# Kernel tuning notes

Measured on AMD Instinct MI355X. Metric: run time of the kernel, lower is better.

## Reference

```python
import jax, jax.numpy as jnp
import numpy as np

TWO_PI = 2.0 * np.pi
SIGMA = 25.0  # marginal_prob_std sigma


def marginal_prob_std(t):
    # std(t) = sqrt((sigma^{2t} - 1) / (2 ln sigma)) for VE-SDE
    return jnp.sqrt((SIGMA ** (2.0 * t) - 1.0) / (2.0 * np.log(SIGMA)))


def edge_conv(x, src, dst, W1, b1, W2, b2, num_nodes):
    # PyG EdgeConv: msg = mlp(cat([x_i, x_j - x_i])), x_i = x[dst], x_j = x[src];
    # scatter-max over dst. First linear split so concat is never materialized:
    # cat([x_i, x_j - x_i]) @ W1 = x_i @ (Wa - Wb) + x_j @ Wb
    d = x.shape[-1]
    Wa, Wb = W1[:d], W1[d:]
    h_center = x @ (Wa - Wb)        # [N, H]
    h_nbr = x @ Wb                  # [N, H]
    e = jax.nn.relu(h_center[dst] + h_nbr[src] + b1)  # [E, H]
    e = e @ W2 + b2                 # [E, out]
    return jax.ops.segment_max(e, dst, num_segments=num_nodes)


def setup_inputs() -> dict:
    N, E, B, H, EM = 50000, 500000, 1024, 128, 64
    CLS, SD, GD, WD = 10, 4, 2, 2
    key = jax.random.key(0)
    ks = jax.random.split(key, 32)

    def lin(k, fi, fo):
        return jax.random.normal(k, (fi, fo), jnp.float32) / np.sqrt(fi)

    inp = {
        "t": jax.random.uniform(ks[0], (N, 1), jnp.float32, 1e-3, 1.0),
        "obj_x": jax.random.normal(ks[1], (N, SD), jnp.float32),
        "obj_geo": jax.random.normal(ks[2], (N, GD), jnp.float32),
        "wall": jax.random.normal(ks[3], (B, WD), jnp.float32),
        "category": jax.random.randint(ks[4], (N,), 0, CLS),
        "batch_idx": jnp.sort(jax.random.randint(ks[5], (N,), 0, B)),
        "src": jax.random.randint(ks[6], (E,), 0, N),
        "dst": jnp.tile(jnp.arange(N), E // N),  # every node receives edges
        "embed_W": jax.random.normal(ks[7], (CLS, EM), jnp.float32),
        "gfp_W": jax.random.normal(ks[8], (EM // 2,), jnp.float32) * 30.0,
        "sW": lin(ks[9], EM, EM), "sb": jnp.zeros((EM,), jnp.float32),
        "w1": lin(ks[10], WD, EM), "wb1": jnp.zeros((EM,), jnp.float32),
        "w2": lin(ks[11], EM, EM), "wb2": jnp.zeros((EM,), jnp.float32),
        "i1": lin(ks[12], SD + GD, H), "ib1": jnp.zeros((H,), jnp.float32),
        "i2": lin(ks[13], H, H), "ib2": jnp.zeros((H,), jnp.float32),
        "m1W1": lin(ks[14], 2 * (H + 3 * EM), H), "m1b1": jnp.zeros((H,), jnp.float32),
        "m1W2": lin(ks[15], H, H), "m1b2": jnp.zeros((H,), jnp.float32),
        "m2W1": lin(ks[16], 2 * (H + 3 * EM), H), "m2b1": jnp.zeros((H,), jnp.float32),
        "m2W2": lin(ks[17], H, SD), "m2b2": jnp.zeros((SD,), jnp.float32),
    }
    return inp


def reference(t, obj_x, obj_geo, wall, category, batch_idx, src, dst,
              embed_W, gfp_W, sW, sb, w1, wb1, w2, wb2,
              i1, ib1, i2, ib2, m1W1, m1b1, m1W2, m1b2,
              m2W1, m2b1, m2W2, m2b2):
    N = obj_x.shape[0]
    # conditioning features
    class_feat = jax.nn.relu(embed_W[category])                       # [N, EM]
    tv = t[:, 0]                                                      # [N]
    x_proj = tv[:, None] * gfp_W[None, :] * TWO_PI                    # [N, EM/2]
    gfp = jnp.concatenate([jnp.sin(x_proj), jnp.cos(x_proj)], axis=-1)
    sigma_feat = jax.nn.relu(gfp @ sW + sb)                           # [N, EM]
    wall_h = jax.nn.relu(jax.nn.relu(wall @ w1 + wb1) @ w2 + wb2)     # [B, EM]
    wall_feat = wall_h[batch_idx]                                     # [N, EM]
    cond = jnp.concatenate([class_feat, sigma_feat, wall_feat], axis=-1)

    # init encoder
    xin = jnp.concatenate([obj_x, obj_geo], axis=-1)                  # [N, 6]
    init = jax.nn.relu(jax.nn.relu(xin @ i1 + ib1) @ i2 + ib2)        # [N, H]

    # main backbone: two EdgeConvs with conditioning concat
    x = jnp.concatenate([init, cond], axis=-1)                        # [N, H+3EM]
    x = jax.nn.relu(edge_conv(x, src, dst, m1W1, m1b1, m1W2, m1b2, N))
    x = jnp.concatenate([x, cond], axis=-1)                           # [N, H+3EM]
    x = edge_conv(x, src, dst, m2W1, m2b1, m2W2, m2b2, N)             # [N, 4]

    return x / (marginal_prob_std(t) + 1e-7)
```

## Files before the change

kernel.cpp:

```cpp
#include <hip/hip_runtime.h>
#include <math.h>

#define NTHREADS 256
#define TWO_PI_F 6.28318530717958647692f
#define LOG_SIGMA 3.2188758248682006f

typedef unsigned short u16;
typedef unsigned int u32;
typedef _Float16 f16x2 __attribute__((ext_vector_type(2)));
typedef _Float16 f16x8 __attribute__((ext_vector_type(8)));
typedef float f32x4 __attribute__((ext_vector_type(4)));

#define MFMA16(a, b, c) __builtin_amdgcn_mfma_f32_16x16x32_f16((a), (b), (c), 0, 0, 0)

__device__ __forceinline__ u16 f2h(float f) {
  _Float16 h = (_Float16)f;
  union { _Float16 h; u16 u; } cv;
  cv.h = h;
  return cv.u;
}
__device__ __forceinline__ f16x2 relu2(f16x2 x) {
  f16x2 z;
  z[0] = (_Float16)0.f; z[1] = (_Float16)0.f;
  return __builtin_elementwise_max(x, z);
}

__global__ __launch_bounds__(256) void prep_kernel(
    const float* __restrict__ m1W2, const float* __restrict__ m1W1,
    const float* __restrict__ m2W1, const float* __restrict__ sW,
    const float* __restrict__ i1, const float* __restrict__ i2,
    const float* __restrict__ m2W2,
    u16* __restrict__ m1W2t, u16* __restrict__ Wc1t, u16* __restrict__ Wc2t,
    u16* __restrict__ sWt, u16* __restrict__ i1t, u16* __restrict__ i2t,
    u16* __restrict__ m2W2t) {
  int idx = blockIdx.x * 256 + threadIdx.x;
  if (idx < 16384) {
    int n = idx >> 7, k = idx & 127;
    m1W2t[idx] = f2h(m1W2[k * 128 + n]);
  } else if (idx < 98304) {
    int j = idx - 16384;
    int n = j / 320, k = j - n * 320;
    float v = (n < 128) ? (m1W1[k * 128 + n] - m1W1[(320 + k) * 128 + n])
                        : m1W1[(320 + k) * 128 + (n - 128)];
    Wc1t[j] = f2h(v);
  } else if (idx < 180224) {
    int j = idx - 98304;
    int n = j / 320, k = j - n * 320;
    float v = (n < 128) ? (m2W1[k * 128 + n] - m2W1[(320 + k) * 128 + n])
                        : m2W1[(320 + k) * 128 + (n - 128)];
    Wc2t[j] = f2h(v);
  } else if (idx < 184320) {
    int j = idx - 180224;
    int n = j >> 6, k = j & 63;
    sWt[j] = f2h(sW[k * 64 + n]);
  } else if (idx < 188416) {
    int j = idx - 184320;
    int n = j >> 5, k = j & 31;
    i1t[j] = (k < 6) ? f2h(i1[k * 128 + n]) : (u16)0;
  } else if (idx < 204800) {
    int j = idx - 188416;
    int n = j >> 7, k = j & 127;
    i2t[j] = f2h(i2[k * 128 + n]);
  } else if (idx < 205312) {
    int j = idx - 204800;
    int n = j >> 7, k = j & 127;
    m2W2t[j] = f2h(m2W2[k * 4 + n]);
  }
}

__global__ void wall_kernel(const float* __restrict__ wall,
                            const float* __restrict__ w1, const float* __restrict__ wb1,
                            const float* __restrict__ w2, const float* __restrict__ wb2,
                            float* __restrict__ wall_h) {
  __shared__ float h1[64];
  int b = blockIdx.x;
  int f = threadIdx.x;
  float v = wall[b * 2 + 0] * w1[f] + wall[b * 2 + 1] * w1[64 + f] + wb1[f];
  h1[f] = fmaxf(v, 0.f);
  __syncthreads();
  float acc = wb2[f];
  for (int k = 0; k < 64; ++k) acc = fmaf(h1[k], w2[k * 64 + f], acc);
  wall_h[b * 64 + f] = fmaxf(acc, 0.f);
}

__global__ __launch_bounds__(256) void node_kernel(
    const float* __restrict__ t, const float* __restrict__ obj_x,
    const float* __restrict__ obj_geo,
    const int* __restrict__ category, const int* __restrict__ batch_idx,
    const float* __restrict__ embed_W, const float* __restrict__ gfp_W,
    const u16* __restrict__ sWt, const float* __restrict__ sb,
    const u16* __restrict__ i1t, const float* __restrict__ ib1,
    const u16* __restrict__ i2t, const float* __restrict__ ib2,
    const u16* __restrict__ Wc1t, const float* __restrict__ m1b1,
    const float* __restrict__ wall_h,
    u16* __restrict__ hc1f, u16* __restrict__ hn1f,
    u16* __restrict__ cond_h, int N) {
  __shared__ u16 xb[64 * 328];
  __shared__ u16 ab[64 * 136];
  __shared__ float t_s[64];
  __shared__ int cat_s[64];
  __shared__ int bid_s[64];

  const int tid = threadIdx.x;
  const int base = blockIdx.x * 64;
  const int wave = tid >> 6, lane = tid & 63;
  const int ln16 = lane & 15, q8 = lane >> 4;

  f16x8 bs0 = *(const f16x8*)(sWt + (size_t)((wave * 16 + ln16) * 64) + q8 * 8);
  f16x8 bs1 = *(const f16x8*)(sWt + (size_t)((wave * 16 + ln16) * 64) + 32 + q8 * 8);
  f16x8 bh[2];
#pragma unroll
  for (int nt = 0; nt < 2; ++nt)
    bh[nt] = *(const f16x8*)(i1t + (size_t)((wave * 32 + nt * 16 + ln16) * 32) + q8 * 8);

  if (tid < 64) {
    int node = min(base + tid, N - 1);
    t_s[tid] = t[node];
    cat_s[tid] = category[node];
    bid_s[tid] = batch_idx[node];
  }
  __syncthreads();

  for (int idx = tid; idx < 64 * 32; idx += NTHREADS) {
    int row = idx >> 5, k = idx & 31;
    float xp = t_s[row] * gfp_W[k] * TWO_PI_F;
    float s, c;
    sincosf(xp, &s, &c);
    ab[row * 136 + k] = f2h(s);
    ab[row * 136 + 32 + k] = f2h(c);
  }
  for (int idx = tid; idx < 64 * 64; idx += NTHREADS) {
    int row = idx >> 6, f = idx & 63;
    xb[row * 328 + 128 + f] = f2h(fmaxf(embed_W[cat_s[row] * 64 + f], 0.f));
    xb[row * 328 + 256 + f] = f2h(wall_h[bid_s[row] * 64 + f]);
  }
  __syncthreads();

  f32x4 cs[4];
#pragma unroll
  for (int mt = 0; mt < 4; ++mt) cs[mt] = (f32x4)0.f;
#pragma unroll
  for (int mt = 0; mt < 4; ++mt) {
    f16x8 a0 = *(const f16x8*)&ab[(mt * 16 + ln16) * 136 + q8 * 8];
    cs[mt] = MFMA16(a0, bs0, cs[mt]);
  }
#pragma unroll
  for (int mt = 0; mt < 4; ++mt) {
    f16x8 a1 = *(const f16x8*)&ab[(mt * 16 + ln16) * 136 + 32 + q8 * 8];
    cs[mt] = MFMA16(a1, bs1, cs[mt]);
  }
  __syncthreads();

  {
    int col = wave * 16 + ln16;
    float bias = sb[col];
#pragma unroll
    for (int mt = 0; mt < 4; ++mt)
#pragma unroll
      for (int r = 0; r < 4; ++r)
        xb[(mt * 16 + q8 * 4 + r) * 328 + 192 + col] = f2h(fmaxf(cs[mt][r] + bias, 0.f));
  }
  for (int idx = tid; idx < 64 * 32; idx += NTHREADS) {
    int row = idx >> 5, k = idx & 31;
    int node = min(base + row, N - 1);
    float v = (k < 4) ? obj_x[node * 4 + k] : ((k < 6) ? obj_geo[node * 2 + (k - 4)] : 0.f);
    ab[row * 136 + k] = f2h(v);
  }
  __syncthreads();

  for (int idx = tid; idx < 64 * 24; idx += NTHREADS) {
    int row = idx / 24, q = idx - row * 24;
    int node = base + row;
    if (node < N)
      *(uint4*)&cond_h[(size_t)node * 192 + q * 8] = *(uint4*)&xb[row * 328 + 128 + q * 8];
  }

  f32x4 ch[2][4];
#pragma unroll
  for (int nt = 0; nt < 2; ++nt)
#pragma unroll
    for (int mt = 0; mt < 4; ++mt) ch[nt][mt] = (f32x4)0.f;
#pragma unroll
  for (int mt = 0; mt < 4; ++mt) {
    f16x8 a = *(const f16x8*)&ab[(mt * 16 + ln16) * 136 + q8 * 8];
#pragma unroll
    for (int nt = 0; nt < 2; ++nt) ch[nt][mt] = MFMA16(a, bh[nt], ch[nt][mt]);
  }
  f16x8 bcur2[2], bnext2[2];
#pragma unroll
  for (int nt = 0; nt < 2; ++nt)
    bcur2[nt] = *(const f16x8*)(i2t + (size_t)((wave * 32 + nt * 16 + ln16) * 128) + q8 * 8);
  __syncthreads();
#pragma unroll
  for (int nt = 0; nt < 2; ++nt) {
    int col = wave * 32 + nt * 16 + ln16;
    float bias = ib1[col];
#pragma unroll
    for (int mt = 0; mt < 4; ++mt)
#pragma unroll
      for (int r = 0; r < 4; ++r)
        ab[(mt * 16 + q8 * 4 + r) * 136 + col] = f2h(fmaxf(ch[nt][mt][r] + bias, 0.f));
  }
  __syncthreads();

  f32x4 ci[2][4];
#pragma unroll
  for (int nt = 0; nt < 2; ++nt)
#pragma unroll
    for (int mt = 0; mt < 4; ++mt) ci[nt][mt] = (f32x4)0.f;
  for (int kt = 0; kt < 4; ++kt) {
    if (kt < 3) {
#pragma unroll
      for (int nt = 0; nt < 2; ++nt)
        bnext2[nt] = *(const f16x8*)(i2t + (size_t)((wave * 32 + nt * 16 + ln16) * 128) +
                                     (kt + 1) * 32 + q8 * 8);
    }
#pragma unroll
    for (int mt = 0; mt < 4; ++mt) {
      f16x8 a = *(const f16x8*)&ab[(mt * 16 + ln16) * 136 + kt * 32 + q8 * 8];
#pragma unroll
      for (int nt = 0; nt < 2; ++nt) ci[nt][mt] = MFMA16(a, bcur2[nt], ci[nt][mt]);
    }
#pragma unroll
    for (int nt = 0; nt < 2; ++nt) bcur2[nt] = bnext2[nt];
  }
#pragma unroll
  for (int nt = 0; nt < 2; ++nt) {
    int col = wave * 32 + nt * 16 + ln16;
    float bias = ib2[col];
#pragma unroll
    for (int mt = 0; mt < 4; ++mt)
#pragma unroll
      for (int r = 0; r < 4; ++r)
        xb[(mt * 16 + q8 * 4 + r) * 328 + col] = f2h(fmaxf(ci[nt][mt][r] + bias, 0.f));
  }
  __syncthreads();

  f32x4 c2[4][4];
#pragma unroll
  for (int nt = 0; nt < 4; ++nt)
#pragma unroll
    for (int mt = 0; mt < 4; ++mt) c2[nt][mt] = (f32x4)0.f;
  f16x8 bcur[4], bnext[4];
#pragma unroll
  for (int nt = 0; nt < 4; ++nt)
    bcur[nt] = *(const f16x8*)(Wc1t + (size_t)((wave * 64 + nt * 16 + ln16) * 320) + q8 * 8);
  for (int kt = 0; kt < 10; ++kt) {
    if (kt < 9) {
#pragma unroll
      for (int nt = 0; nt < 4; ++nt)
        bnext[nt] = *(const f16x8*)(Wc1t + (size_t)((wave * 64 + nt * 16 + ln16) * 320) +
                                    (kt + 1) * 32 + q8 * 8);
    }
#pragma unroll
    for (int mt = 0; mt < 4; ++mt) {
      f16x8 a = *(const f16x8*)&xb[(mt * 16 + ln16) * 328 + kt * 32 + q8 * 8];
#pragma unroll
      for (int nt = 0; nt < 4; ++nt) c2[nt][mt] = MFMA16(a, bcur[nt], c2[nt][mt]);
    }
#pragma unroll
    for (int nt = 0; nt < 4; ++nt) bcur[nt] = bnext[nt];
  }
#pragma unroll
  for (int nt = 0; nt < 4; ++nt) {
    int col = wave * 64 + nt * 16 + ln16;
#pragma unroll
    for (int mt = 0; mt < 4; ++mt)
#pragma unroll
      for (int r = 0; r < 4; ++r) {
        int node = base + mt * 16 + q8 * 4 + r;
        if (node < N) {
          if (col < 128)
            hc1f[(size_t)node * 128 + col] = f2h(c2[nt][mt][r] + m1b1[col]);
          else
            hn1f[(size_t)node * 128 + (col - 128)] = f2h(c2[nt][mt][r]);
        }
      }
  }
}

__global__ __launch_bounds__(256) void edge1_kernel(
    const u16* __restrict__ hc1f, const u16* __restrict__ hn1f,
    const int* __restrict__ src, const u16* __restrict__ m1W2t,
    const float* __restrict__ m1b2, u16* __restrict__ y, int N) {
  __shared__ int sid[320];
  const int tid = threadIdx.x;
  const int base = blockIdx.x * 32;
  const int wave = tid >> 6, lane = tid & 63;
  const int ln16 = lane & 15, q8 = lane >> 4;
  const int rowoff = (wave >> 1) * 16;
  const int colh = (wave & 1) * 64;
  const int myrow = rowoff + ln16;
  const int mynode = min(base + myrow, N - 1);

  for (int idx = tid; idx < 320; idx += NTHREADS) {
    int e = idx >> 5, n = idx & 31;
    sid[idx] = src[min(base + n, N - 1) + e * N];
  }

  uint4 hc4[4];
#pragma unroll
  for (int kt = 0; kt < 4; ++kt)
    hc4[kt] = *(const uint4*)&hc1f[(size_t)mynode * 128 + kt * 32 + q8 * 8];

  f16x8 bfr[4][4];
#pragma unroll
  for (int nt = 0; nt < 4; ++nt)
#pragma unroll
    for (int kt = 0; kt < 4; ++kt)
      bfr[nt][kt] = *(const f16x8*)(m1W2t + (size_t)(colh + nt * 16 + ln16) * 128 +
                                    kt * 32 + q8 * 8);
  __syncthreads();

  f32x4 ymax[4];
#pragma unroll
  for (int nt = 0; nt < 4; ++nt)
#pragma unroll
    for (int r = 0; r < 4; ++r) ymax[nt][r] = -3.0e38f;

  uint4 g[2][4];
  {
    int s0 = sid[myrow];
    int s1 = sid[32 + myrow];
#pragma unroll
    for (int kt = 0; kt < 4; ++kt) {
      g[0][kt] = *(const uint4*)&hn1f[(size_t)s0 * 128 + kt * 32 + q8 * 8];
      g[1][kt] = *(const uint4*)&hn1f[(size_t)s1 * 128 + kt * 32 + q8 * 8];
    }
  }
#pragma unroll
  for (int e = 0; e < 10; ++e) {
    const int sl = e & 1;
    uint4 a4[4];
#pragma unroll
    for (int kt = 0; kt < 4; ++kt) {
      f16x2* ap = (f16x2*)&a4[kt];
      const f16x2* gp = (const f16x2*)&g[sl][kt];
      const f16x2* hp = (const f16x2*)&hc4[kt];
#pragma unroll
      for (int p = 0; p < 4; ++p) ap[p] = relu2(gp[p] + hp[p]);
    }
    if (e + 2 < 10) {
      int s = sid[(e + 2) * 32 + myrow];
#pragma unroll
      for (int kt = 0; kt < 4; ++kt)
        g[sl][kt] = *(const uint4*)&hn1f[(size_t)s * 128 + kt * 32 + q8 * 8];
    }
    f32x4 c[4];
#pragma unroll
    for (int nt = 0; nt < 4; ++nt) c[nt] = (f32x4)0.f;
#pragma unroll
    for (int kt = 0; kt < 4; ++kt) {
      f16x8 a = *(const f16x8*)&a4[kt];
#pragma unroll
      for (int nt = 0; nt < 4; ++nt) c[nt] = MFMA16(a, bfr[nt][kt], c[nt]);
    }
#pragma unroll
    for (int nt = 0; nt < 4; ++nt)
#pragma unroll
      for (int r = 0; r < 4; ++r) ymax[nt][r] = fmaxf(ymax[nt][r], c[nt][r]);
  }

#pragma unroll
  for (int nt = 0; nt < 4; ++nt) {
    int col = colh + nt * 16 + ln16;
    float bias = m1b2[col];
#pragma unroll
    for (int r = 0; r < 4; ++r) {
      int node = base + rowoff + q8 * 4 + r;
      if (node < N) y[(size_t)node * 128 + col] = f2h(fmaxf(ymax[nt][r] + bias, 0.f));
    }
  }
}

__global__ __launch_bounds__(256) void conv2_kernel(
    const u16* __restrict__ y, const u16* __restrict__ cond_h,
    const u16* __restrict__ Wc2t, const float* __restrict__ m2b1,
    u16* __restrict__ hc2f, u16* __restrict__ hn2f, int N) {
  __shared__ u16 xb[64 * 328];
  const int tid = threadIdx.x;
  const int base = blockIdx.x * 64;
  const int wave = tid >> 6, lane = tid & 63;
  const int ln16 = lane & 15, q8 = lane >> 4;

  for (int idx = tid; idx < 64 * 16; idx += NTHREADS) {
    int row = idx >> 4, q = idx & 15;
    int nd = min(base + row, N - 1);
    *(uint4*)&xb[row * 328 + q * 8] = *(const uint4*)&y[(size_t)nd * 128 + q * 8];
  }
  for (int idx = tid; idx < 64 * 24; idx += NTHREADS) {
    int row = idx / 24, q = idx - row * 24;
    int nd = min(base + row, N - 1);
    *(uint4*)&xb[row * 328 + 128 + q * 8] = *(const uint4*)&cond_h[(size_t)nd * 192 + q * 8];
  }
  __syncthreads();

  f32x4 c2[4][4];
#pragma unroll
  for (int nt = 0; nt < 4; ++nt)
#pragma unroll
    for (int mt = 0; mt < 4; ++mt) c2[nt][mt] = (f32x4)0.f;
  f16x8 bcur[4], bnext[4];
#pragma unroll
  for (int nt = 0; nt < 4; ++nt)
    bcur[nt] = *(const f16x8*)(Wc2t + (size_t)((wave * 64 + nt * 16 + ln16) * 320) + q8 * 8);
  for (int kt = 0; kt < 10; ++kt) {
    if (kt < 9) {
#pragma unroll
      for (int nt = 0; nt < 4; ++nt)
        bnext[nt] = *(const f16x8*)(Wc2t + (size_t)((wave * 64 + nt * 16 + ln16) * 320) +
                                    (kt + 1) * 32 + q8 * 8);
    }
#pragma unroll
    for (int mt = 0; mt < 4; ++mt) {
      f16x8 a = *(const f16x8*)&xb[(mt * 16 + ln16) * 328 + kt * 32 + q8 * 8];
#pragma unroll
      for (int nt = 0; nt < 4; ++nt) c2[nt][mt] = MFMA16(a, bcur[nt], c2[nt][mt]);
    }
#pragma unroll
    for (int nt = 0; nt < 4; ++nt) bcur[nt] = bnext[nt];
  }
#pragma unroll
  for (int nt = 0; nt < 4; ++nt) {
    int col = wave * 64 + nt * 16 + ln16;
#pragma unroll
    for (int mt = 0; mt < 4; ++mt)
#pragma unroll
      for (int r = 0; r < 4; ++r) {
        int node = base + mt * 16 + q8 * 4 + r;
        if (node < N) {
          if (col < 128)
            hc2f[(size_t)node * 128 + col] = f2h(c2[nt][mt][r] + m2b1[col]);
          else
            hn2f[(size_t)node * 128 + (col - 128)] = f2h(c2[nt][mt][r]);
        }
      }
  }
}

__global__ __launch_bounds__(256) void edge2_kernel(
    const u16* __restrict__ hc2f, const u16* __restrict__ hn2f,
    const int* __restrict__ src, const float* __restrict__ t,
    const u16* __restrict__ m2W2t, const float* __restrict__ m2b2,
    float* __restrict__ out, int N) {
  const int tid = threadIdx.x;
  const int base = blockIdx.x * 32;
  const int ln = tid >> 3, kq = tid & 7;
  const int node = min(base + ln, N - 1);

  uint4 hc0 = *(const uint4*)&hc2f[(size_t)node * 128 + kq * 16];
  uint4 hc1_ = *(const uint4*)&hc2f[(size_t)node * 128 + kq * 16 + 8];
  uint4 w4[4][2];
#pragma unroll
  for (int j = 0; j < 4; ++j) {
    w4[j][0] = *(const uint4*)&m2W2t[j * 128 + kq * 16];
    w4[j][1] = *(const uint4*)&m2W2t[j * 128 + kq * 16 + 8];
  }
  float ymax[4] = {-3.0e38f, -3.0e38f, -3.0e38f, -3.0e38f};

  uint4 g[2][2];
  {
    int s0 = src[node];
    int s1 = src[node + N];
    g[0][0] = *(const uint4*)&hn2f[(size_t)s0 * 128 + kq * 16];
    g[0][1] = *(const uint4*)&hn2f[(size_t)s0 * 128 + kq * 16 + 8];
    g[1][0] = *(const uint4*)&hn2f[(size_t)s1 * 128 + kq * 16];
    g[1][1] = *(const uint4*)&hn2f[(size_t)s1 * 128 + kq * 16 + 8];
  }
#pragma unroll
  for (int e = 0; e < 10; ++e) {
    const int sl = e & 1;
    f16x2 a2[8];
    {
      const f16x2* gp0 = (const f16x2*)&g[sl][0];
      const f16x2* gp1 = (const f16x2*)&g[sl][1];
      const f16x2* hp0 = (const f16x2*)&hc0;
      const f16x2* hp1 = (const f16x2*)&hc1_;
#pragma unroll
      for (int p = 0; p < 4; ++p) a2[p] = relu2(gp0[p] + hp0[p]);
#pragma unroll
      for (int p = 0; p < 4; ++p) a2[4 + p] = relu2(gp1[p] + hp1[p]);
    }
    if (e + 2 < 10) {
      int s = src[node + (e + 2) * N];
      g[sl][0] = *(const uint4*)&hn2f[(size_t)s * 128 + kq * 16];
      g[sl][1] = *(const uint4*)&hn2f[(size_t)s * 128 + kq * 16 + 8];
    }
    float acc[4] = {0.f, 0.f, 0.f, 0.f};
#pragma unroll
    for (int j = 0; j < 4; ++j) {
      const f16x2* wp0 = (const f16x2*)&w4[j][0];
      const f16x2* wp1 = (const f16x2*)&w4[j][1];
#pragma unroll
      for (int p = 0; p < 4; ++p) {
        acc[j] = __builtin_amdgcn_fdot2(a2[p], wp0[p], acc[j], false);
        acc[j] = __builtin_amdgcn_fdot2(a2[4 + p], wp1[p], acc[j], false);
      }
    }
#pragma unroll
    for (int mask = 1; mask <= 4; mask <<= 1)
#pragma unroll
      for (int j = 0; j < 4; ++j) acc[j] += __shfl_xor(acc[j], mask);
#pragma unroll
    for (int j = 0; j < 4; ++j) ymax[j] = fmaxf(ymax[j], acc[j]);
  }
  if (kq < 4 && base + ln < N) {
    float tv = t[node];
    float mps = sqrtf((expf(2.f * tv * LOG_SIGMA) - 1.f) * (1.f / (2.f * LOG_SIGMA)));
    out[(size_t)node * 4 + kq] = (ymax[kq] + m2b2[kq]) / (mps + 1e-7f);
  }
}

extern "C" void kernel_launch(void* const* d_in, const int* in_sizes, int n_in,
                              void* d_out, int out_size, void* d_ws, size_t ws_size,
                              hipStream_t stream) {
  const float* t = (const float*)d_in[0];
  const float* obj_x = (const float*)d_in[1];
  const float* obj_geo = (const float*)d_in[2];
  const float* wall = (const float*)d_in[3];
  const int* category = (const int*)d_in[4];
  const int* batch_idx = (const int*)d_in[5];
  const int* src = (const int*)d_in[6];
  const float* embed_W = (const float*)d_in[8];
  const float* gfp_W = (const float*)d_in[9];
  const float* sW = (const float*)d_in[10];
  const float* sb = (const float*)d_in[11];
  const float* w1 = (const float*)d_in[12];
  const float* wb1 = (const float*)d_in[13];
  const float* w2 = (const float*)d_in[14];
  const float* wb2 = (const float*)d_in[15];
  const float* i1 = (const float*)d_in[16];
  const float* ib1 = (const float*)d_in[17];
  const float* i2 = (const float*)d_in[18];
  const float* ib2 = (const float*)d_in[19];
  const float* m1W1 = (const float*)d_in[20];
  const float* m1b1 = (const float*)d_in[21];
  const float* m1W2 = (const float*)d_in[22];
  const float* m1b2 = (const float*)d_in[23];
  const float* m2W1 = (const float*)d_in[24];
  const float* m2b1 = (const float*)d_in[25];
  const float* m2W2 = (const float*)d_in[26];
  const float* m2b2 = (const float*)d_in[27];
  float* out = (float*)d_out;

  const int N = in_sizes[0];
  const int B = in_sizes[3] / 2;

  char* w = (char*)d_ws;
  float* wall_h = (float*)w; w += (size_t)B * 64 * 4;
  u16* cond_h = (u16*)w;    w += (size_t)N * 192 * 2;
  u16* hc1f = (u16*)w;      w += (size_t)N * 128 * 2;
  u16* hn1f = (u16*)w;      w += (size_t)N * 128 * 2;
  u16* hc2f = (u16*)w;      w += (size_t)N * 128 * 2;
  u16* hn2f = (u16*)w;      w += (size_t)N * 128 * 2;
  u16* yb = (u16*)w;        w += (size_t)N * 128 * 2;
  u16* m1W2t = (u16*)w;     w += (size_t)128 * 128 * 2;
  u16* Wc1t = (u16*)w;      w += (size_t)256 * 320 * 2;
  u16* Wc2t = (u16*)w;      w += (size_t)256 * 320 * 2;
  u16* sWt = (u16*)w;       w += (size_t)64 * 64 * 2;
  u16* i1t = (u16*)w;       w += (size_t)128 * 32 * 2;
  u16* i2t = (u16*)w;       w += (size_t)128 * 128 * 2;
  u16* m2W2t = (u16*)w;     w += (size_t)4 * 128 * 2;

  prep_kernel<<<dim3(802), dim3(256), 0, stream>>>(m1W2, m1W1, m2W1, sW, i1, i2, m2W2,
                                                   m1W2t, Wc1t, Wc2t, sWt, i1t, i2t, m2W2t);
  wall_kernel<<<dim3(B), dim3(64), 0, stream>>>(wall, w1, wb1, w2, wb2, wall_h);
  node_kernel<<<dim3((N + 63) / 64), dim3(NTHREADS), 0, stream>>>(
      t, obj_x, obj_geo, category, batch_idx, embed_W, gfp_W, sWt, sb,
      i1t, ib1, i2t, ib2, Wc1t, m1b1, wall_h, hc1f, hn1f, cond_h, N);
  edge1_kernel<<<dim3((N + 31) / 32), dim3(NTHREADS), 0, stream>>>(
      hc1f, hn1f, src, m1W2t, m1b2, yb, N);
  conv2_kernel<<<dim3((N + 63) / 64), dim3(NTHREADS), 0, stream>>>(
      yb, cond_h, Wc2t, m2b1, hc2f, hn2f, N);
  edge2_kernel<<<dim3((N + 31) / 32), dim3(NTHREADS), 0, stream>>>(
      hc2f, hn2f, src, t, m2W2t, m2b2, out, N);
}
```

Before: 332.6 us.

## Use MFMA in edge2 and retile edge1 to 16 nodes per block

Edge2's per-edge 128x4 projection moves from fdot2 with cross-lane shuffle reductions to a 16x16x32 MFMA. The weights are zero-padded to 16 output columns and the source indices are staged in shared memory for 64 nodes per block. Edge1 now handles 16 nodes per block, with each wave owning 32 output columns, and both kernels get a launch_bounds occupancy hint. This cuts shuffle and VALU work and raises occupancy. The costs are wasted MFMA columns in edge2 and each hn1f gathered row being loaded by all four waves in edge1.

After: 359.4 us. +8.1%, slower.

```diff
diff --git a/kernel.cpp b/kernel.cpp
--- a/kernel.cpp
+++ b/kernel.cpp
@@ -61,10 +61,10 @@
     int j = idx - 188416;
     int n = j >> 7, k = j & 127;
     i2t[j] = f2h(i2[k * 128 + n]);
-  } else if (idx < 205312) {
+  } else if (idx < 206848) {
     int j = idx - 204800;
     int n = j >> 7, k = j & 127;
-    m2W2t[j] = f2h(m2W2[k * 4 + n]);
+    m2W2t[j] = (n < 4) ? f2h(m2W2[k * 4 + n]) : (u16)0;
   }
 }
 
@@ -279,22 +279,19 @@
   }
 }
 
-__global__ __launch_bounds__(256) void edge1_kernel(
+__global__ __launch_bounds__(256, 4) void edge1_kernel(
     const u16* __restrict__ hc1f, const u16* __restrict__ hn1f,
     const int* __restrict__ src, const u16* __restrict__ m1W2t,
     const float* __restrict__ m1b2, u16* __restrict__ y, int N) {
-  __shared__ int sid[320];
+  __shared__ int sid[160];
   const int tid = threadIdx.x;
-  const int base = blockIdx.x * 32;
+  const int base = blockIdx.x * 16;
   const int wave = tid >> 6, lane = tid & 63;
   const int ln16 = lane & 15, q8 = lane >> 4;
-  const int rowoff = (wave >> 1) * 16;
-  const int colh = (wave & 1) * 64;
-  const int myrow = rowoff + ln16;
-  const int mynode = min(base + myrow, N - 1);
-
-  for (int idx = tid; idx < 320; idx += NTHREADS) {
-    int e = idx >> 5, n = idx & 31;
+  const int mynode = min(base + ln16, N - 1);
+
+  for (int idx = tid; idx < 160; idx += NTHREADS) {
+    int e = idx >> 4, n = idx & 15;
     sid[idx] = src[min(base + n, N - 1) + e * N];
   }
 
@@ -303,25 +300,25 @@
   for (int kt = 0; kt < 4; ++kt)
     hc4[kt] = *(const uint4*)&hc1f[(size_t)mynode * 128 + kt * 32 + q8 * 8];
 
-  f16x8 bfr[4][4];
-#pragma unroll
-  for (int nt = 0; nt < 4; ++nt)
+  f16x8 bfr[2][4];
+#pragma unroll
+  for (int nt = 0; nt < 2; ++nt)
 #pragma unroll
     for (int kt = 0; kt < 4; ++kt)
-      bfr[nt][kt] = *(const f16x8*)(m1W2t + (size_t)(colh + nt * 16 + ln16) * 128 +
+      bfr[nt][kt] = *(const f16x8*)(m1W2t + (size_t)(wave * 32 + nt * 16 + ln16) * 128 +
                                     kt * 32 + q8 * 8);
   __syncthreads();
 
-  f32x4 ymax[4];
-#pragma unroll
-  for (int nt = 0; nt < 4; ++nt)
+  f32x4 ymax[2];
+#pragma unroll
+  for (int nt = 0; nt < 2; ++nt)
 #pragma unroll
     for (int r = 0; r < 4; ++r) ymax[nt][r] = -3.0e38f;
 
   uint4 g[2][4];
   {
-    int s0 = sid[myrow];
-    int s1 = sid[32 + myrow];
+    int s0 = sid[ln16];
+    int s1 = sid[16 + ln16];
 #pragma unroll
     for (int kt = 0; kt < 4; ++kt) {
       g[0][kt] = *(const uint4*)&hn1f[(size_t)s0 * 128 + kt * 32 + q8 * 8];
@@ -341,33 +338,33 @@
       for (int p = 0; p < 4; ++p) ap[p] = relu2(gp[p] + hp[p]);
     }
     if (e + 2 < 10) {
-      int s = sid[(e + 2) * 32 + myrow];
+      int s = sid[(e + 2) * 16 + ln16];
 #pragma unroll
       for (int kt = 0; kt < 4; ++kt)
         g[sl][kt] = *(const uint4*)&hn1f[(size_t)s * 128 + kt * 32 + q8 * 8];
     }
-    f32x4 c[4];
-#pragma unroll
-    for (int nt = 0; nt < 4; ++nt) c[nt] = (f32x4)0.f;
+    f32x4 c[2];
+#pragma unroll
+    for (int nt = 0; nt < 2; ++nt) c[nt] = (f32x4)0.f;
 #pragma unroll
     for (int kt = 0; kt < 4; ++kt) {
       f16x8 a = *(const f16x8*)&a4[kt];
 #pragma unroll
-      for (int nt = 0; nt < 4; ++nt) c[nt] = MFMA16(a, bfr[nt][kt], c[nt]);
-    }
-#pragma unroll
-    for (int nt = 0; nt < 4; ++nt)
+      for (int nt = 0; nt < 2; ++nt) c[nt] = MFMA16(a, bfr[nt][kt], c[nt]);
+    }
+#pragma unroll
+    for (int nt = 0; nt < 2; ++nt)
 #pragma unroll
       for (int r = 0; r < 4; ++r) ymax[nt][r] = fmaxf(ymax[nt][r], c[nt][r]);
   }
 
 #pragma unroll
-  for (int nt = 0; nt < 4; ++nt) {
-    int col = colh + nt * 16 + ln16;
+  for (int nt = 0; nt < 2; ++nt) {
+    int col = wave * 32 + nt * 16 + ln16;
     float bias = m1b2[col];
 #pragma unroll
     for (int r = 0; r < 4; ++r) {
-      int node = base + rowoff + q8 * 4 + r;
+      int node = base + q8 * 4 + r;
       if (node < N) y[(size_t)node * 128 + col] = f2h(fmaxf(ymax[nt][r] + bias, 0.f));
     }
   }
@@ -438,76 +435,88 @@
   }
 }
 
-__global__ __launch_bounds__(256) void edge2_kernel(
+__global__ __launch_bounds__(256, 4) void edge2_kernel(
     const u16* __restrict__ hc2f, const u16* __restrict__ hn2f,
     const int* __restrict__ src, const float* __restrict__ t,
     const u16* __restrict__ m2W2t, const float* __restrict__ m2b2,
     float* __restrict__ out, int N) {
+  __shared__ int sid[640];
   const int tid = threadIdx.x;
-  const int base = blockIdx.x * 32;
-  const int ln = tid >> 3, kq = tid & 7;
-  const int node = min(base + ln, N - 1);
-
-  uint4 hc0 = *(const uint4*)&hc2f[(size_t)node * 128 + kq * 16];
-  uint4 hc1_ = *(const uint4*)&hc2f[(size_t)node * 128 + kq * 16 + 8];
-  uint4 w4[4][2];
-#pragma unroll
-  for (int j = 0; j < 4; ++j) {
-    w4[j][0] = *(const uint4*)&m2W2t[j * 128 + kq * 16];
-    w4[j][1] = *(const uint4*)&m2W2t[j * 128 + kq * 16 + 8];
-  }
-  float ymax[4] = {-3.0e38f, -3.0e38f, -3.0e38f, -3.0e38f};
-
-  uint4 g[2][2];
+  const int base = blockIdx.x * 64;
+  const int wave = tid >> 6, lane = tid & 63;
+  const int ln16 = lane & 15, q8 = lane >> 4;
+  const int myrow = wave * 16 + ln16;
+  const int mynode = min(base + myrow, N - 1);
+
+  for (int idx = tid; idx < 640; idx += NTHREADS) {
+    int e = idx >> 6, n = idx & 63;
+    sid[idx] = src[min(base + n, N - 1) + e * N];
+  }
+
+  uint4 hc4[4];
+#pragma unroll
+  for (int kt = 0; kt < 4; ++kt)
+    hc4[kt] = *(const uint4*)&hc2f[(size_t)mynode * 128 + kt * 32 + q8 * 8];
+
+  f16x8 bfr[4];
+#pragma unroll
+  for (int kt = 0; kt < 4; ++kt)
+    bfr[kt] = *(const f16x8*)(m2W2t + (size_t)ln16 * 128 + kt * 32 + q8 * 8);
+  __syncthreads();
+
+  f32x4 ymax;
+#pragma unroll
+  for (int r = 0; r < 4; ++r) ymax[r] = -3.0e38f;
+
+  uint4 g[2][4];
   {
-    int s0 = src[node];
-    int s1 = src[node + N];
-    g[0][0] = *(const uint4*)&hn2f[(size_t)s0 * 128 + kq * 16];
-    g[0][1] = *(const uint4*)&hn2f[(size_t)s0 * 128 + kq * 16 + 8];
-    g[1][0] = *(const uint4*)&hn2f[(size_t)s1 * 128 + kq * 16];
-    g[1][1] = *(const uint4*)&hn2f[(size_t)s1 * 128 + kq * 16 + 8];
+    int s0 = sid[myrow];
+    int s1 = sid[64 + myrow];
+#pragma unroll
+    for (int kt = 0; kt < 4; ++kt) {
+      g[0][kt] = *(const uint4*)&hn2f[(size_t)s0 * 128 + kt * 32 + q8 * 8];
+      g[1][kt] = *(const uint4*)&hn2f[(size_t)s1 * 128 + kt * 32 + q8 * 8];
+    }
   }
 #pragma unroll
   for (int e = 0; e < 10; ++e) {
     const int sl = e & 1;
-    f16x2 a2[8];
-    {
-      const f16x2* gp0 = (const f16x2*)&g[sl][0];
-      const f16x2* gp1 = (const f16x2*)&g[sl][1];
-      const f16x2* hp0 = (const f16x2*)&hc0;
-      const f16x2* hp1 = (const f16x2*)&hc1_;
-#pragma unroll
-      for (int p = 0; p < 4; ++p) a2[p] = relu2(gp0[p] + hp0[p]);
-#pragma unroll
-      for (int p = 0; p < 4; ++p) a2[4 + p] = relu2(gp1[p] + hp1[p]);
+    uint4 a4[4];
+#pragma unroll
+    for (int kt = 0; kt < 4; ++kt) {
+      f16x2* ap = (f16x2*)&a4[kt];
+      const f16x2* gp = (const f16x2*)&g[sl][kt];
+      const f16x2* hp = (const f16x2*)&hc4[kt];
+#pragma unroll
+      for (int p = 0; p < 4; ++p) ap[p] = relu2(gp[p] + hp[p]);
     }
     if (e + 2 < 10) {
-      int s = src[node + (e + 2) * N];
-      g[sl][0] = *(const uint4*)&hn2f[(size_t)s * 128 + kq * 16];
-      g[sl][1] = *(const uint4*)&hn2f[(size_t)s * 128 + kq * 16 + 8];
-    }
-    float acc[4] = {0.f, 0.f, 0.f, 0.f};
-#pragma unroll
-    for (int j = 0; j < 4; ++j) {
-      const f16x2* wp0 = (const f16x2*)&w4[j][0];
-      const f16x2* wp1 = (const f16x2*)&w4[j][1];
-#pragma unroll
-      for (int p = 0; p < 4; ++p) {
-        acc[j] = __builtin_amdgcn_fdot2(a2[p], wp0[p], acc[j], false);
-        acc[j] = __builtin_amdgcn_fdot2(a2[4 + p], wp1[p], acc[j], false);
+      int s = sid[(e + 2) * 64 + myrow];
+#pragma unroll
+      for (int kt = 0; kt < 4; ++kt)
+        g[sl][kt] = *(const uint4*)&hn2f[(size_t)s * 128 + kt * 32 + q8 * 8];
+    }
+    f32x4 c = (f32x4)0.f;
+#pragma unroll
+    for (int kt = 0; kt < 4; ++kt) {
+      f16x8 a = *(const f16x8*)&a4[kt];
+      c = MFMA16(a, bfr[kt], c);
+    }
+#pragma unroll
+    for (int r = 0; r < 4; ++r) ymax[r] = fmaxf(ymax[r], c[r]);
+  }
+
+  if (ln16 < 4) {
+    float bias = m2b2[ln16];
+#pragma unroll
+    for (int r = 0; r < 4; ++r) {
+      int node = base + wave * 16 + q8 * 4 + r;
+      if (node < N) {
+        float tv = t[node];
+        float mps = sqrtf((expf(2.f * tv * LOG_SIGMA) - 1.f) * (1.f / (2.f * LOG_SIGMA)));
+        out[(size_t)node * 4 + ln16] = (ymax[r] + bias) / (mps + 1e-7f);
       }
     }
-#pragma unroll
-    for (int mask = 1; mask <= 4; mask <<= 1)
-#pragma unroll
-      for (int j = 0; j < 4; ++j) acc[j] += __shfl_xor(acc[j], mask);
-#pragma unroll
-    for (int j = 0; j < 4; ++j) ymax[j] = fmaxf(ymax[j], acc[j]);
-  }
-  if (kq < 4 && base + ln < N) {
-    float tv = t[node];
-    float mps = sqrtf((expf(2.f * tv * LOG_SIGMA) - 1.f) * (1.f / (2.f * LOG_SIGMA)));
-    out[(size_t)node * 4 + kq] = (ymax[kq] + m2b2[kq]) / (mps + 1e-7f);
   }
 }
 
@@ -560,18 +569,18 @@
   u16* sWt = (u16*)w;       w += (size_t)64 * 64 * 2;
   u16* i1t = (u16*)w;       w += (size_t)128 * 32 * 2;
   u16* i2t = (u16*)w;       w += (size_t)128 * 128 * 2;
-  u16* m2W2t = (u16*)w;     w += (size_t)4 * 128 * 2;
-
-  prep_kernel<<<dim3(802), dim3(256), 0, stream>>>(m1W2, m1W1, m2W1, sW, i1, i2, m2W2,
+  u16* m2W2t = (u16*)w;     w += (size_t)16 * 128 * 2;
+
+  prep_kernel<<<dim3(808), dim3(256), 0, stream>>>(m1W2, m1W1, m2W1, sW, i1, i2, m2W2,
                                                    m1W2t, Wc1t, Wc2t, sWt, i1t, i2t, m2W2t);
   wall_kernel<<<dim3(B), dim3(64), 0, stream>>>(wall, w1, wb1, w2, wb2, wall_h);
   node_kernel<<<dim3((N + 63) / 64), dim3(NTHREADS), 0, stream>>>(
       t, obj_x, obj_geo, category, batch_idx, embed_W, gfp_W, sWt, sb,
       i1t, ib1, i2t, ib2, Wc1t, m1b1, wall_h, hc1f, hn1f, cond_h, N);
-  edge1_kernel<<<dim3((N + 31) / 32), dim3(NTHREADS), 0, stream>>>(
+  edge1_kernel<<<dim3((N + 15) / 16), dim3(NTHREADS), 0, stream>>>(
       hc1f, hn1f, src, m1W2t, m1b2, yb, N);
   conv2_kernel<<<dim3((N + 63) / 64), dim3(NTHREADS), 0, stream>>>(
       yb, cond_h, Wc2t, m2b1, hc2f, hn2f, N);
-  edge2_kernel<<<dim3((N + 31) / 32), dim3(NTHREADS), 0, stream>>>(
+  edge2_kernel<<<dim3((N + 63) / 64), dim3(NTHREADS), 0, stream>>>(
       hc2f, hn2f, src, t, m2W2t, m2b2, out, N);
 }
```
